# Optimization experiments

Hardware: AMD Instinct MI355X
Metric: run time of the kernel (lower is better)

## Reference

```python
import jax, jax.numpy as jnp
import numpy as np

B, N_USERS, N_ITEMS, E, UF, IF = 1024, 1000, 1000, 128, 32, 32
IN_SIZE = E + UF + E + IF  # 320
EPS = 1e-12


def _gru_zero_hidden(x, w_ih, b_ih, b_hh):
    # PyTorch GRUCell with hx=None (zeros): h' = (1-z)*n
    gi = x @ w_ih.T + b_ih                      # (B, 3E)
    i_r, i_z, i_n = jnp.split(gi, 3, axis=1)
    h_r, h_z, h_n = jnp.split(b_hh, 3)
    r = jax.nn.sigmoid(i_r + h_r)
    z = jax.nn.sigmoid(i_z + h_z)
    n = jnp.tanh(i_n + r * h_n)
    return (1.0 - z) * n


def _l2_normalize(x):
    nrm = jnp.sqrt(jnp.sum(x * x, axis=1, keepdims=True))
    return x / jnp.maximum(nrm, EPS)


def setup_inputs() -> dict:
    key = jax.random.key(0)
    ks = jax.random.split(key, 10)
    uid = jax.random.randint(ks[0], (B,), 0, N_USERS)
    iid = jax.random.randint(ks[1], (B,), 0, N_ITEMS)
    feats = jax.random.normal(ks[2], (B, UF + IF), dtype=jnp.float32)
    inputs = jnp.concatenate([uid[:, None].astype(jnp.float32), iid[:, None].astype(jnp.float32), feats], axis=1)
    s = 0.05
    return {
        "inputs": inputs,
        "user_memory": jax.random.normal(ks[3], (B, N_USERS, E), dtype=jnp.float32),
        "item_memory": jax.random.normal(ks[4], (B, N_ITEMS, E), dtype=jnp.float32),
        "w_ih_u": jax.random.normal(ks[5], (3 * E, IN_SIZE), dtype=jnp.float32) * s,
        "b_ih_u": jnp.zeros((3 * E,), dtype=jnp.float32),
        "b_hh_u": jnp.zeros((3 * E,), dtype=jnp.float32),
        "w_ih_i": jax.random.normal(ks[6], (3 * E, IN_SIZE), dtype=jnp.float32) * s,
        "b_ih_i": jnp.zeros((3 * E,), dtype=jnp.float32),
        "b_hh_i": jnp.zeros((3 * E,), dtype=jnp.float32),
    }


def reference(inputs, user_memory, item_memory, w_ih_u, b_ih_u, b_hh_u, w_ih_i, b_ih_i, b_hh_i):
    b = jnp.arange(B)
    user_ids = inputs[:, 0].astype(jnp.int32)
    item_ids = inputs[:, 1].astype(jnp.int32)
    user_features = inputs[:, 2:2 + UF]
    item_features = inputs[:, 2 + UF:]
    # gather per-batch-row memory slots
    um = user_memory[b, user_ids]               # (B, E)
    im = item_memory[b, item_ids]               # (B, E)
    user_inputs = jnp.concatenate([um, user_features, im, item_features], axis=1)
    item_inputs = jnp.concatenate([im, item_features, um, user_features], axis=1)
    new_u = _gru_zero_hidden(user_inputs, w_ih_u, b_ih_u, b_hh_u)
    new_i = _gru_zero_hidden(item_inputs, w_ih_i, b_ih_i, b_hh_i)
    new_u = _l2_normalize(new_u)
    new_i = _l2_normalize(new_i)
    # scatter back into memories
    user_memory = user_memory.at[b, user_ids].set(new_u)
    item_memory = item_memory.at[b, item_ids].set(new_i)
    out = jnp.concatenate([user_ids[:, None].astype(jnp.float32), item_ids[:, None].astype(jnp.float32), new_u, new_i], axis=1)
    return out, user_memory, item_memory
```

## Files before the change

kernel.cpp:

```cpp
#include <hip/hip_runtime.h>
#include <math.h>

#define BATCH 1024
#define NU 1000
#define NI 1000
#define EDIM 128
#define INROW 66
#define IN_SIZE 320
#define OUTROW 258
#define G 4

typedef float f32x4 __attribute__((ext_vector_type(4)));

__global__ __launch_bounds__(256) void limnet_compute(
    const float* __restrict__ inputs,
    const float* __restrict__ umem,
    const float* __restrict__ imem,
    const float* __restrict__ w_u, const float* __restrict__ bih_u, const float* __restrict__ bhh_u,
    const float* __restrict__ w_i, const float* __restrict__ bih_i, const float* __restrict__ bhh_i,
    float* __restrict__ out,
    float* __restrict__ udst, float* __restrict__ idst)
{
    __shared__ float xx[G][640];
    __shared__ float gi[G][768];
    __shared__ float psum[4][G];
    __shared__ int   ids[G][2];

    const int t = threadIdx.x;
    const int wave = t >> 6, lane = t & 63;
    const int lane16 = lane & 15, sub = lane >> 4;
    const int b0 = blockIdx.x * G;

    for (int g = 0; g < G; ++g) {
        const int b = b0 + g;
        const float* inrow = inputs + (long)b * INROW;
        const int uid = (int)inrow[0];
        const int iid = (int)inrow[1];
        if (t == 0) { ids[g][0] = uid; ids[g][1] = iid; }
        if (t < 128) {
            float v = umem[((long)b * NU + uid) * EDIM + t];
            xx[g][t]       = v;  xx[g][320 + t] = v;
            float w = imem[((long)b * NI + iid) * EDIM + t];
            xx[g][160 + t] = w;  xx[g][480 + t] = w;
        } else {
            int s = t - 128;
            if (s < 32)      { float v = inrow[2 + s];  xx[g][128 + s] = v; xx[g][448 + s] = v; }
            else if (s < 64) { int s2 = s - 32; float v = inrow[34 + s2]; xx[g][288 + s2] = v; xx[g][608 + s2] = v; }
        }
    }
    __syncthreads();

    const int isItemW = (wave >= 2);
    const int xoff = isItemW ? 160 : 0;
    f32x4 xv[G][5];
    #pragma unroll
    for (int g = 0; g < G; ++g)
        #pragma unroll
        for (int i = 0; i < 5; ++i)
            xv[g][i] = *(const f32x4*)&xx[g][xoff + lane16 * 4 + i * 64];

    const float* wbase = isItemW ? w_i : w_u;
    const int rbase = (wave & 1) * 192;
    const int gibase = isItemW ? 384 : 0;
    for (int it = 0; it < 48; ++it) {
        const int row = rbase + it * 4 + sub;
        const float* wrow = wbase + (long)row * IN_SIZE;
        float acc[G] = {0.f, 0.f, 0.f, 0.f};
        #pragma unroll
        for (int i = 0; i < 5; ++i) {
            const f32x4 wv = *(const f32x4*)&wrow[lane16 * 4 + i * 64];
            #pragma unroll
            for (int g = 0; g < G; ++g)
                acc[g] += wv.x * xv[g][i].x + wv.y * xv[g][i].y
                        + wv.z * xv[g][i].z + wv.w * xv[g][i].w;
        }
        #pragma unroll
        for (int off = 8; off >= 1; off >>= 1) {
            #pragma unroll
            for (int g = 0; g < G; ++g) acc[g] += __shfl_xor(acc[g], off);
        }
        if (lane16 == 0) {
            #pragma unroll
            for (int g = 0; g < G; ++g) gi[g][gibase + row] = acc[g];
        }
    }
    __syncthreads();

    const int isItem = (t >= 128);
    const int d = isItem ? (t - 128) : t;
    const float* bih = isItem ? bih_i : bih_u;
    const float* bhh = isItem ? bhh_i : bhh_u;
    const float br = bih[d]       + bhh[d];
    const float bz = bih[128 + d] + bhh[128 + d];
    const float bn = bih[256 + d];
    const float hn = bhh[256 + d];
    const int gib = isItem ? 384 : 0;

    float val[G], ss[G];
    #pragma unroll
    for (int g = 0; g < G; ++g) {
        float ir  = gi[g][gib + d];
        float iz  = gi[g][gib + 128 + d];
        float inn = gi[g][gib + 256 + d];
        float r = 1.f / (1.f + expf(-(ir + br)));
        float z = 1.f / (1.f + expf(-(iz + bz)));
        float n = tanhf(inn + bn + r * hn);
        val[g] = (1.f - z) * n;
        ss[g]  = val[g] * val[g];
    }
    #pragma unroll
    for (int off = 32; off >= 1; off >>= 1) {
        #pragma unroll
        for (int g = 0; g < G; ++g) ss[g] += __shfl_xor(ss[g], off);
    }
    if (lane == 0) {
        #pragma unroll
        for (int g = 0; g < G; ++g) psum[wave][g] = ss[g];
    }
    __syncthreads();

    #pragma unroll
    for (int g = 0; g < G; ++g) {
        float s = isItem ? (psum[2][g] + psum[3][g]) : (psum[0][g] + psum[1][g]);
        float denom = fmaxf(sqrtf(s), 1e-12f);
        float nv = val[g] / denom;
        const int b = b0 + g;
        out[(long)b * OUTROW + 2 + (isItem ? 128 : 0) + d] = nv;
        if (isItem) idst[((long)b * NI + ids[g][1]) * EDIM + d] = nv;
        else        udst[((long)b * NU + ids[g][0]) * EDIM + d] = nv;
    }
    if (t < 2 * G) {
        int g = t >> 1, col = t & 1;
        out[(long)(b0 + g) * OUTROW + col] = (float)ids[g][col];
    }
}

extern "C" void kernel_launch(void* const* d_in, const int* in_sizes, int n_in,
                              void* d_out, int out_size, void* d_ws, size_t ws_size,
                              hipStream_t stream) {
    const float* inputs = (const float*)d_in[0];
    const float* umem   = (const float*)d_in[1];
    const float* imem   = (const float*)d_in[2];
    const float* w_u    = (const float*)d_in[3];
    const float* bih_u  = (const float*)d_in[4];
    const float* bhh_u  = (const float*)d_in[5];
    const float* w_i    = (const float*)d_in[6];
    const float* bih_i  = (const float*)d_in[7];
    const float* bhh_i  = (const float*)d_in[8];
    float* out = (float*)d_out;

    const long OUTSEC = (long)BATCH * OUTROW;
    const long MEMSZ  = (long)BATCH * NU * EDIM;
    float* udst = out + OUTSEC;
    float* idst = out + OUTSEC + MEMSZ;

    hipMemcpyAsync(udst, umem, MEMSZ * sizeof(float),
                   hipMemcpyDeviceToDevice, stream);
    hipMemcpyAsync(idst, imem, MEMSZ * sizeof(float),
                   hipMemcpyDeviceToDevice, stream);

    limnet_compute<<<BATCH / G, 256, 0, stream>>>(
        inputs, umem, imem, w_u, bih_u, bhh_u, w_i, bih_i, bhh_i,
        out, udst, idst);
}
```

Measured before the change: 450.5 us.

## Fuse memory copy into compute kernel with nontemporal vector copies

Replaces the two device-to-device memcpys with copy blocks inside the compute kernel, using nontemporal 16-byte loads and stores and skipping the rows that the compute blocks will overwrite. This removes the separate copy launches and serialization, and lets the GRU compute overlap with the bandwidth-bound copy. The shared input buffer is also halved by reading the item-side input through rotated offsets, and x values are read from LDS inside the loop instead of being held in registers. The risks are extra LDS reads in the inner loop and a copy path that may reach lower bandwidth than the runtime memcpy.

```diff
diff --git a/kernel.cpp b/kernel.cpp
--- a/kernel.cpp
+++ b/kernel.cpp
@@ -9,10 +9,12 @@
 #define IN_SIZE 320
 #define OUTROW 258
 #define G 4
+#define NCOMPUTE 256
+#define NCOPY 10240
 
 typedef float f32x4 __attribute__((ext_vector_type(4)));
 
-__global__ __launch_bounds__(256) void limnet_compute(
+__global__ __launch_bounds__(256, 8) void limnet_fused(
     const float* __restrict__ inputs,
     const float* __restrict__ umem,
     const float* __restrict__ imem,
@@ -21,15 +23,36 @@
     float* __restrict__ out,
     float* __restrict__ udst, float* __restrict__ idst)
 {
-    __shared__ float xx[G][640];
+    __shared__ float xx[G][320];
     __shared__ float gi[G][768];
     __shared__ float psum[4][G];
     __shared__ int   ids[G][2];
 
+    const int bid = blockIdx.x;
     const int t = threadIdx.x;
+
+    if (bid >= NCOMPUTE) {
+        const int cb0 = bid - NCOMPUTE;
+        const int item = cb0 >= 5120;
+        const int cb = cb0 - item * 5120;
+        const int b = cb / 5;
+        const f32x4* __restrict__ src = (const f32x4*)(item ? imem : umem);
+        f32x4* __restrict__ dst = (f32x4*)(item ? idst : udst);
+        const int id = (int)inputs[(long)b * INROW + item];
+        const int skiprow = b * 1000 + id;
+        long p = (long)cb * 6400 + t;
+        #pragma unroll 5
+        for (int i = 0; i < 25; ++i, p += 256) {
+            f32x4 v = __builtin_nontemporal_load(&src[p]);
+            if ((int)(p >> 5) != skiprow)
+                __builtin_nontemporal_store(v, &dst[p]);
+        }
+        return;
+    }
+
     const int wave = t >> 6, lane = t & 63;
     const int lane16 = lane & 15, sub = lane >> 4;
-    const int b0 = blockIdx.x * G;
+    const int b0 = bid * G;
 
     for (int g = 0; g < G; ++g) {
         const int b = b0 + g;
@@ -38,30 +61,27 @@
         const int iid = (int)inrow[1];
         if (t == 0) { ids[g][0] = uid; ids[g][1] = iid; }
         if (t < 128) {
-            float v = umem[((long)b * NU + uid) * EDIM + t];
-            xx[g][t]       = v;  xx[g][320 + t] = v;
-            float w = imem[((long)b * NI + iid) * EDIM + t];
-            xx[g][160 + t] = w;  xx[g][480 + t] = w;
-        } else {
-            int s = t - 128;
-            if (s < 32)      { float v = inrow[2 + s];  xx[g][128 + s] = v; xx[g][448 + s] = v; }
-            else if (s < 64) { int s2 = s - 32; float v = inrow[34 + s2]; xx[g][288 + s2] = v; xx[g][608 + s2] = v; }
+            xx[g][t]       = umem[((long)b * NU + uid) * EDIM + t];
+            xx[g][160 + t] = imem[((long)b * NI + iid) * EDIM + t];
+        } else if (t < 160) {
+            int s = t - 128; xx[g][128 + s] = inrow[2 + s];
+        } else if (t < 192) {
+            int s = t - 160; xx[g][288 + s] = inrow[34 + s];
         }
     }
     __syncthreads();
 
     const int isItemW = (wave >= 2);
-    const int xoff = isItemW ? 160 : 0;
-    f32x4 xv[G][5];
-    #pragma unroll
-    for (int g = 0; g < G; ++g)
-        #pragma unroll
-        for (int i = 0; i < 5; ++i)
-            xv[g][i] = *(const f32x4*)&xx[g][xoff + lane16 * 4 + i * 64];
-
     const float* wbase = isItemW ? w_i : w_u;
     const int rbase = (wave & 1) * 192;
     const int gibase = isItemW ? 384 : 0;
+    int xoffs[5];
+    #pragma unroll
+    for (int i = 0; i < 5; ++i) {
+        int o = lane16 * 4 + i * 64;
+        if (isItemW) { o += 160; if (o >= 320) o -= 320; }
+        xoffs[i] = o;
+    }
     for (int it = 0; it < 48; ++it) {
         const int row = rbase + it * 4 + sub;
         const float* wrow = wbase + (long)row * IN_SIZE;
@@ -70,9 +90,10 @@
         for (int i = 0; i < 5; ++i) {
             const f32x4 wv = *(const f32x4*)&wrow[lane16 * 4 + i * 64];
             #pragma unroll
-            for (int g = 0; g < G; ++g)
-                acc[g] += wv.x * xv[g][i].x + wv.y * xv[g][i].y
-                        + wv.z * xv[g][i].z + wv.w * xv[g][i].w;
+            for (int g = 0; g < G; ++g) {
+                const f32x4 xv = *(const f32x4*)&xx[g][xoffs[i]];
+                acc[g] += wv.x * xv.x + wv.y * xv.y + wv.z * xv.z + wv.w * xv.w;
+            }
         }
         #pragma unroll
         for (int off = 8; off >= 1; off >>= 1) {
@@ -154,12 +175,7 @@
     float* udst = out + OUTSEC;
     float* idst = out + OUTSEC + MEMSZ;
 
-    hipMemcpyAsync(udst, umem, MEMSZ * sizeof(float),
-                   hipMemcpyDeviceToDevice, stream);
-    hipMemcpyAsync(idst, imem, MEMSZ * sizeof(float),
-                   hipMemcpyDeviceToDevice, stream);
-
-    limnet_compute<<<BATCH / G, 256, 0, stream>>>(
+    limnet_fused<<<NCOMPUTE + NCOPY, 256, 0, stream>>>(
         inputs, umem, imem, w_u, bih_u, bhh_u, w_i, bih_i, bhh_i,
         out, udst, idst);
 }
```

Measured after the change: 495.7 us. 1.1x slower.
